# Kernel tuning notes

Hardware: AMD Instinct MI355X
Metric: run time of the kernel (lower is better)

Reference implementation:

```python
import jax, jax.numpy as jnp
import numpy as np

L = 1024       # qlen
B = 2          # batch
D = 1024       # hidden_size
NH = 16        # heads
DH = 64        # d_head
NL = 4         # num_hidden_layers
MLEN = 1024    # memory length
KLEN = MLEN + L


def setup_inputs() -> dict:
    key = jax.random.key(0)
    ks = jax.random.split(key, 10)
    s = 0.02
    # causal mask: key position j is masked (True) if j > mlen + i
    attn_mask = (jnp.arange(KLEN)[None, :] > (MLEN + jnp.arange(L))[:, None])[:, :, None]
    return {
        "mems": jax.random.normal(ks[0], (NL + 1, MLEN, B, D), jnp.float32),
        "raw_embeddings": jax.random.normal(ks[1], (L, B, D), jnp.float32),
        "attention_mask": attn_mask,
        "r_w_bias": jax.random.normal(ks[2], (NH, DH), jnp.float32) * s,
        "r_r_bias": jax.random.normal(ks[3], (NH, DH), jnp.float32) * s,
        "qkv_w": jax.random.normal(ks[4], (NL, D, 3 * NH * DH), jnp.float32) * s,
        "r_w": jax.random.normal(ks[5], (NL, D, NH * DH), jnp.float32) * s,
        "o_w": jax.random.normal(ks[6], (NL, NH * DH, D), jnp.float32) * s,
        "ln1_g": jnp.ones((NL, D), jnp.float32),
        "ln1_b": jnp.zeros((NL, D), jnp.float32),
        "ff_w1": jax.random.normal(ks[7], (NL, D, D), jnp.float32) * s,
        "ff_b1": jnp.zeros((NL, D), jnp.float32),
        "ff_w2": jax.random.normal(ks[8], (NL, D, D), jnp.float32) * s,
        "ff_b2": jnp.zeros((NL, D), jnp.float32),
        "ln2_g": jnp.ones((NL, D), jnp.float32),
        "ln2_b": jnp.zeros((NL, D), jnp.float32),
    }


def _layernorm(x, g, b, eps=1e-5):
    m = jnp.mean(x, axis=-1, keepdims=True)
    v = jnp.var(x, axis=-1, keepdims=True)
    return (x - m) / jnp.sqrt(v + eps) * g + b


def _rel_shift(x):
    # x: (qlen, rlen, b, n) -> XL relative shift via pad/reshape trick
    q, r, b, n = x.shape
    xp = jnp.pad(x, ((0, 0), (1, 0), (0, 0), (0, 0)))     # (q, r+1, b, n)
    xp = xp.reshape(r + 1, q, b, n)                        # flat reinterpret
    return xp[1:].reshape(q, r, b, n)


def _forward(mems, raw_embeddings, attention_mask, r_w_bias, r_r_bias, qkv_w, r_w,
             o_w, ln1_g, ln1_b, ff_w1, ff_b1, ff_w2, ff_b2, ln2_g, ln2_b):
    qlen, bsz, d = raw_embeddings.shape
    mlen = mems.shape[1]
    klen = mlen + qlen
    nh, dh = r_w_bias.shape
    scale = 1.0 / (dh ** 0.5)

    # sinusoidal relative positional embedding: pos_seq = klen-1 ... 0
    pos_seq = jnp.arange(klen - 1, -1, -1, dtype=raw_embeddings.dtype)
    inv_freq = 1.0 / (10000.0 ** (jnp.arange(0, d, 2, dtype=jnp.float32) / d))
    sinusoid = pos_seq[:, None] * inv_freq[None, :]
    pos_emb = jnp.concatenate([jnp.sin(sinusoid), jnp.cos(sinusoid)], axis=-1)  # (klen, D)

    mask = attention_mask[:, :, :, None]  # (L, 2L, 1, 1)
    core = raw_embeddings
    hids = [core]
    n_layers = qkv_w.shape[0]
    for i in range(n_layers):
        cat = jnp.concatenate([mems[i], core], axis=0)          # (klen, b, D)
        w_heads = cat @ qkv_w[i]                                # (klen, b, 3D)
        q, k, v = jnp.split(w_heads, 3, axis=-1)
        q = q[-qlen:]
        q = q.reshape(qlen, bsz, nh, dh)
        k = k.reshape(klen, bsz, nh, dh)
        v = v.reshape(klen, bsz, nh, dh)
        r_head_k = (pos_emb @ r_w[i]).reshape(klen, nh, dh)     # (rlen, n, d)

        AC = jnp.einsum('ibnd,jbnd->ijbn', q + r_w_bias, k)
        BD = _rel_shift(jnp.einsum('ibnd,jnd->ijbn', q + r_r_bias, r_head_k))
        score = (AC + BD) * scale                               # (q, k, b, n)
        score = jnp.where(mask, -jnp.inf, score)
        prob = jax.nn.softmax(score, axis=1)
        attn_vec = jnp.einsum('ijbn,jbnd->ibnd', prob, v).reshape(qlen, bsz, nh * dh)
        attn_out = attn_vec @ o_w[i]
        core = _layernorm(core + attn_out, ln1_g[i], ln1_b[i])  # post-lnorm

        ff = jnp.maximum(core @ ff_w1[i] + ff_b1[i], 0.0) @ ff_w2[i] + ff_b2[i]
        core = _layernorm(core + ff, ln2_g[i], ln2_b[i])
        hids.append(core)

    new_mems = jax.lax.stop_gradient(jnp.stack(hids, axis=0))   # xl_grad=False -> detach
    return core, new_mems


def reference(mems, raw_embeddings, attention_mask, r_w_bias, r_r_bias, qkv_w, r_w,
              o_w, ln1_g, ln1_b, ff_w1, ff_b1, ff_w2, ff_b2, ln2_g, ln2_b):
    return _forward(mems, raw_embeddings, attention_mask, r_w_bias, r_r_bias, qkv_w,
                    r_w, o_w, ln1_g, ln1_b, ff_w1, ff_b1, ff_w2, ff_b2, ln2_g, ln2_b)
```

## Files before the change

### kernel.cpp

```cpp
#include <hip/hip_runtime.h>
#include <hip/hip_bf16.h>

#define QLEN 1024
#define BSZ 2
#define DIM 1024
#define NH 16
#define DH 64
#define NL 4
#define MLEN 1024
#define KLEN 2048
#define QROWS (QLEN*BSZ)
#define CATROWS (KLEN*BSZ)
#define N3 (3*NH*DH)

typedef __hip_bfloat16 bf16;
typedef short bf16x8_t __attribute__((ext_vector_type(8)));
typedef float f32x4_t __attribute__((ext_vector_type(4)));

__device__ __forceinline__ float b2f(bf16 h) { return __bfloat162float(h); }
__device__ __forceinline__ bf16 f2b(float f) { return __float2bfloat16(f); }
__device__ __forceinline__ short f2bs(float f) {
  bf16 h = f2b(f);
  return *reinterpret_cast<short*>(&h);
}

__device__ __forceinline__ float loadf(const void* p, size_t i, int isb) {
  return isb ? b2f(((const bf16*)p)[i]) : ((const float*)p)[i];
}
__device__ __forceinline__ void storef(void* p, size_t i, float v, int isb) {
  if (isb) ((bf16*)p)[i] = f2b(v);
  else     ((float*)p)[i] = v;
}

__device__ __forceinline__ bf16x8_t load_bf8(const bf16* p) {
  union { uint4 u; bf16x8_t v; } x;
  x.u = *reinterpret_cast<const uint4*>(p);
  return x.v;
}

__device__ __forceinline__ void gld_lds16(const bf16* g, bf16* l) {
  __builtin_amdgcn_global_load_lds(
      (const __attribute__((address_space(1))) void*)g,
      (__attribute__((address_space(3))) void*)l, 16, 0, 0);
}

__global__ void probe_kernel(const void* g, int* flag) {
  *flag = (((const unsigned int*)g)[0] == 0x3F803F80u) ? 1 : 0;
}

__global__ void pos_emb_kernel(bf16* __restrict__ pe) {
  int idx = blockIdx.x * 256 + threadIdx.x;
  int j = idx >> 10;
  int c = idx & 1023;
  int fi = (c < 512) ? c : (c - 512);
  float inv = expf(-((float)(2 * fi) * (1.0f / 1024.0f)) * 9.210340371976184f);
  float pos = (float)(KLEN - 1 - j);
  float a = pos * inv;
  float v = (c < 512) ? sinf(a) : cosf(a);
  pe[idx] = f2b(v);
}

__global__ void init_kernel(const void* __restrict__ raw, float* __restrict__ core,
                            void* __restrict__ out, const int* __restrict__ flag) {
  const int isb = *flag;
  int idx = blockIdx.x * 256 + threadIdx.x;
  float v = loadf(raw, idx, isb);
  core[idx] = v;
  storef(out, (size_t)QROWS * DIM + idx, v, isb);
}

__global__ void concat_kernel(const void* __restrict__ mems, size_t memsOff,
                              const float* __restrict__ core,
                              bf16* __restrict__ cat, const int* __restrict__ flag) {
  const int isb = *flag;
  int idx = blockIdx.x * 256 + threadIdx.x;
  const int memElems = MLEN * BSZ * DIM;
  if (idx < memElems) cat[idx] = f2b(loadf(mems, memsOff + idx, isb));
  else                cat[idx] = f2b(core[idx - memElems]);
}

__global__ void transpose5_kernel(const void* __restrict__ qkvw, const void* __restrict__ rw,
                                  const void* __restrict__ ow, const void* __restrict__ ffw1,
                                  const void* __restrict__ ffw2,
                                  bf16* __restrict__ qkvT, bf16* __restrict__ rwT,
                                  bf16* __restrict__ owT, bf16* __restrict__ f1T,
                                  bf16* __restrict__ f2T,
                                  int layer, const int* __restrict__ flag) {
  const int isb = *flag;
  __shared__ float tile[32][33];
  const int n0 = blockIdx.x * 32;
  const int k0 = blockIdx.y * 32;
  const int tx = threadIdx.x & 31;
  const int ty = threadIdx.x >> 5;
  auto doT = [&](const void* W, size_t wOff, bf16* WT, int K, int N) {
    __syncthreads();
#pragma unroll
    for (int r = 0; r < 32; r += 8)
      tile[ty + r][tx] = loadf(W, wOff + (size_t)(k0 + ty + r) * N + n0 + tx, isb);
    __syncthreads();
#pragma unroll
    for (int r = 0; r < 32; r += 8)
      WT[(size_t)(n0 + ty + r) * K + k0 + tx] = f2b(tile[tx][ty + r]);
  };
  doT(qkvw, (size_t)layer * DIM * N3, qkvT, DIM, N3);
  if (n0 < DIM) {
    const size_t o = (size_t)layer * DIM * DIM;
    doT(rw,   o, rwT, DIM, DIM);
    doT(ow,   o, owT, DIM, DIM);
    doT(ffw1, o, f1T, DIM, DIM);
    doT(ffw2, o, f2T, DIM, DIM);
  }
}

template <int EPI, int BM>
__launch_bounds__(256, 2)
__global__ void mgemm_kernel(const bf16* __restrict__ A, const bf16* __restrict__ Bt,
                             float* __restrict__ Cf, bf16* __restrict__ Ch,
                             bf16* __restrict__ Vt,
                             const void* __restrict__ bias, size_t biasOff,
                             int M, int N, int K, const int* __restrict__ flag) {
  const int isb = *flag;
  constexpr int BN = (BM == 128) ? 128 : 64;
  __shared__ bf16 As[BM * 32];
  __shared__ bf16 Bs[BN * 32];
  const int t = threadIdx.x;
  const int wave = t >> 6;
  const int lane = t & 63;
  const int g  = lane >> 4;
  const int lo = lane & 15;
  const int rowA = blockIdx.y * BM;
  const int rowB = blockIdx.x * BN;

  if constexpr (BM == 128) {
    const int wr = wave >> 1, wc = wave & 1;
    const int srow = wave * 32 + (lane >> 2);
    const int scol = (lane & 3) * 8;
    const bf16* gA = A  + (size_t)(rowA + srow) * K + scol;
    const bf16* gB = Bt + (size_t)(rowB + srow) * K + scol;
    bf16* lA = As + wave * 32 * 32;
    bf16* lB = Bs + wave * 32 * 32;

    f32x4_t acc[4][4];
#pragma unroll
    for (int m = 0; m < 4; ++m)
#pragma unroll
      for (int n = 0; n < 4; ++n) acc[m][n] = (f32x4_t){0.f, 0.f, 0.f, 0.f};

    for (int k0 = 0; k0 < K; k0 += 32) {
      gld_lds16(gA + k0, lA);
      gld_lds16(gA + (size_t)16 * K + k0, lA + 16 * 32);
      gld_lds16(gB + k0, lB);
      gld_lds16(gB + (size_t)16 * K + k0, lB + 16 * 32);
      __syncthreads();
      bf16x8_t af[4], bfr[4];
#pragma unroll
      for (int m = 0; m < 4; ++m)
        af[m] = *reinterpret_cast<const bf16x8_t*>(As + (wr * 64 + m * 16 + lo) * 32 + g * 8);
#pragma unroll
      for (int n = 0; n < 4; ++n)
        bfr[n] = *reinterpret_cast<const bf16x8_t*>(Bs + (wc * 64 + n * 16 + lo) * 32 + g * 8);
#pragma unroll
      for (int m = 0; m < 4; ++m)
#pragma unroll
        for (int n = 0; n < 4; ++n)
          acc[m][n] = __builtin_amdgcn_mfma_f32_16x16x32_bf16(af[m], bfr[n], acc[m][n], 0, 0, 0);
      __syncthreads();
    }

#pragma unroll
    for (int m = 0; m < 4; ++m) {
#pragma unroll
      for (int n = 0; n < 4; ++n) {
        const int col = rowB + wc * 64 + n * 16 + lo;
        float bv = 0.f;
        if constexpr (EPI >= 2 && EPI <= 3) bv = loadf(bias, biasOff + col, isb);
#pragma unroll
        for (int r = 0; r < 4; ++r) {
          const int row = rowA + wr * 64 + m * 16 + g * 4 + r;
          float v = acc[m][n][r];
          const size_t o = (size_t)row * N + col;
          if constexpr (EPI == 0)      Cf[o] = v;
          else if constexpr (EPI == 1) Ch[o] = f2b(v);
          else if constexpr (EPI == 2) { v += bv; Ch[o] = f2b(fmaxf(v, 0.f)); }
          else if constexpr (EPI == 3) { v += bv; Cf[o] = v; }
          else {
            if (col < 2 * DIM) Ch[o] = f2b(v);
            else Vt[((size_t)(row & 1) * DIM + (col - 2 * DIM)) * KLEN + (row >> 1)] = f2b(v);
          }
        }
      }
    }
  } else {
    const int srow = t >> 2;
    const int scol = (t & 3) * 8;
    const bf16* gA = A  + (size_t)(rowA + srow) * K + scol;
    const bf16* gB = Bt + (size_t)(rowB + srow) * K + scol;
    bf16* lA = As + wave * 16 * 32;
    bf16* lB = Bs + wave * 16 * 32;

    f32x4_t acc[4];
#pragma unroll
    for (int n = 0; n < 4; ++n) acc[n] = (f32x4_t){0.f, 0.f, 0.f, 0.f};

    for (int k0 = 0; k0 < K; k0 += 32) {
      gld_lds16(gA + k0, lA);
      gld_lds16(gB + k0, lB);
      __syncthreads();
      bf16x8_t af = *reinterpret_cast<const bf16x8_t*>(As + (wave * 16 + lo) * 32 + g * 8);
      bf16x8_t bfr[4];
#pragma unroll
      for (int n = 0; n < 4; ++n)
        bfr[n] = *reinterpret_cast<const bf16x8_t*>(Bs + (n * 16 + lo) * 32 + g * 8);
#pragma unroll
      for (int n = 0; n < 4; ++n)
        acc[n] = __builtin_amdgcn_mfma_f32_16x16x32_bf16(af, bfr[n], acc[n], 0, 0, 0);
      __syncthreads();
    }

#pragma unroll
    for (int n = 0; n < 4; ++n) {
      const int col = rowB + n * 16 + lo;
      float bv = 0.f;
      if constexpr (EPI >= 2) bv = loadf(bias, biasOff + col, isb);
#pragma unroll
      for (int r = 0; r < 4; ++r) {
        const int row = rowA + wave * 16 + g * 4 + r;
        float v = acc[n][r];
        const size_t o = (size_t)row * N + col;
        if constexpr (EPI == 0)      Cf[o] = v;
        else if constexpr (EPI == 1) Ch[o] = f2b(v);
        else if constexpr (EPI == 2) { v += bv; Ch[o] = f2b(fmaxf(v, 0.f)); }
        else if constexpr (EPI == 3) { v += bv; Cf[o] = v; }
      }
    }
  }
}

#define PSTR 56

__launch_bounds__(256)
__global__ void attn_mfma_kernel(const bf16* __restrict__ wh, const bf16* __restrict__ vT,
                                 const bf16* __restrict__ rk,
                                 const void* __restrict__ rwb, const void* __restrict__ rrb,
                                 bf16* __restrict__ av, const int* __restrict__ flag) {
  const int isb = *flag;
  const int bid = blockIdx.x;
  const int x  = bid & 7;
  const int j  = bid >> 3;
  const int head = x * 4 + (j & 3);
  const int b = head >> 4;
  const int n = head & 15;
  const int jj = j >> 2;
  const int qb = (jj < 8) ? jj : 23 - jj;
  const int qbase = qb * 64;
  const int t = threadIdx.x;
  const int wid = t >> 6;
  const int lane = t & 63;
  const int lo = lane & 15;
  const int g  = lane >> 4;
  const int i0 = qbase + wid * 16;

  __shared__ bf16 Kls[2][32 * 64];
  __shared__ bf16 Vtls[2][64 * 32];
  __shared__ bf16 Rls[128 * 64];
  __shared__ short PlsAll[4][16 * PSTR];
  short* Pl = PlsAll[wid];

  const int srow = t >> 3;
  const int kchunk = (t & 7) ^ (srow & 7);
  const size_t rowStride = (size_t)BSZ * N3;
  const bf16* gK  = wh + ((size_t)srow * BSZ + b) * N3 + DIM + n * DH + kchunk * 8;
  const bf16* gVt = vT + ((size_t)b * DIM + n * DH + (t >> 2)) * KLEN
                       + (((t & 3) ^ ((t >> 3) & 3)) << 3);

  auto stageR = [&](int s0) {
    int r = s0 + (t >> 3);
    int rc = (r < KLEN) ? r : (KLEN - 1);
    const bf16* src = rk + (size_t)rc * DIM + n * DH + ((t & 7) ^ ((t >> 3) & 7)) * 8;
    gld_lds16(src, &Rls[(size_t)(s0 & 127) * 64 + (size_t)wid * 512]);
  };

  bf16x8_t qw[2], qr[2];
  {
    const bf16* qrow = wh + ((size_t)(MLEN + i0 + lo) * BSZ + b) * N3 + n * DH;
#pragma unroll
    for (int c = 0; c < 2; ++c) {
      int d0 = c * 32 + g * 8;
#pragma unroll
      for (int jj2 = 0; jj2 < 8; ++jj2) {
        float qv = b2f(qrow[d0 + jj2]);
        qw[c][jj2] = f2bs(qv + loadf(rwb, n * DH + d0 + jj2, isb));
        qr[c][jj2] = f2bs(qv + loadf(rrb, n * DH + d0 + jj2, isb));
      }
    }
  }

  f32x4_t O[4];
  float mrow[4], lrow[4];
#pragma unroll
  for (int d = 0; d < 4; ++d) { O[d] = (f32x4_t){0.f, 0.f, 0.f, 0.f}; }
#pragma unroll
  for (int r = 0; r < 4; ++r) { mrow[r] = -INFINITY; lrow[r] = 0.f; }

  const float SCL = 0.125f * 1.44269504088896f;
  const int jend = MLEN + qbase + 63;

  gld_lds16(gK, &Kls[0][wid * 512]);
  gld_lds16(gVt, &Vtls[0][wid * 512]);
  stageR(MLEN - 64 - qbase);
  stageR(MLEN - 32 - qbase);
  stageR(MLEN - qbase);
  __syncthreads();

  int bi = 0;
  for (int j0 = 0; j0 <= jend; j0 += 32) {
    if (j0 + 32 <= jend) {
      gld_lds16(gK + (size_t)(j0 + 32) * rowStride, &Kls[bi ^ 1][wid * 512]);
      gld_lds16(gVt + j0 + 32, &Vtls[bi ^ 1][wid * 512]);
      stageR(MLEN + 32 + j0 - qbase);
    }
    const bf16* Kl  = Kls[bi];
    const bf16* Vtl = Vtls[bi];

    f32x4_t s[2];
    s[0] = (f32x4_t){0.f, 0.f, 0.f, 0.f};
    s[1] = (f32x4_t){0.f, 0.f, 0.f, 0.f};
#pragma unroll
    for (int c = 0; c < 2; ++c) {
#pragma unroll
      for (int tt = 0; tt < 2; ++tt) {
        const int row = tt * 16 + lo;
        const bf16* kp = Kl + row * 64 + (((c * 4 + g) ^ (row & 7)) << 3);
        s[tt] = __builtin_amdgcn_mfma_f32_16x16x32_bf16(qw[c], load_bf8(kp), s[tt], 0, 0, 0);
      }
    }
    const int u0 = MLEN - 1 + j0 - i0 - 15;
    f32x4_t dacc[3];
    dacc[0] = (f32x4_t){0.f, 0.f, 0.f, 0.f};
    dacc[1] = (f32x4_t){0.f, 0.f, 0.f, 0.f};
    dacc[2] = (f32x4_t){0.f, 0.f, 0.f, 0.f};
#pragma unroll
    for (int c = 0; c < 2; ++c) {
#pragma unroll
      for (int tt = 0; tt < 3; ++tt) {
        const int sr = (u0 + tt * 16 + lo) & 127;
        const bf16* rp = Rls + sr * 64 + (((c * 4 + g) ^ (lo & 7)) << 3);
        dacc[tt] = __builtin_amdgcn_mfma_f32_16x16x32_bf16(qr[c], load_bf8(rp), dacc[tt], 0, 0, 0);
      }
    }

    float sv[2][4];
#pragma unroll
    for (int r = 0; r < 4; ++r) {
      const int ri = g * 4 + r;
      const int srcl = g * 16 + ((lo + 15 - ri) & 15);
      float a0 = __shfl(dacc[0][r], srcl);
      float a1 = __shfl(dacc[1][r], srcl);
      float a2 = __shfl(dacc[2][r], srcl);
      const bool hi = lo > ri;
      float d0 = hi ? a1 : a0;
      float d1 = hi ? a2 : a1;
      bool v0 = (j0 + lo)      <= (MLEN + i0 + ri);
      bool v1 = (j0 + lo + 16) <= (MLEN + i0 + ri);
      sv[0][r] = v0 ? (s[0][r] + d0) * SCL : -INFINITY;
      sv[1][r] = v1 ? (s[1][r] + d1) * SCL : -INFINITY;
    }

    float alpha[4];
#pragma unroll
    for (int r = 0; r < 4; ++r) {
      float v = fmaxf(sv[0][r], sv[1][r]);
      v = fmaxf(v, __shfl_xor(v, 1));
      v = fmaxf(v, __shfl_xor(v, 2));
      v = fmaxf(v, __shfl_xor(v, 4));
      v = fmaxf(v, __shfl_xor(v, 8));
      float mn = fmaxf(mrow[r], v);
      alpha[r] = exp2f(mrow[r] - mn);
      mrow[r] = mn;
    }
    float ps[2][4];
#pragma unroll
    for (int f2 = 0; f2 < 2; ++f2)
#pragma unroll
      for (int r = 0; r < 4; ++r)
        ps[f2][r] = exp2f(sv[f2][r] - mrow[r]);
#pragma unroll
    for (int r = 0; r < 4; ++r) {
      float v = ps[0][r] + ps[1][r];
      v += __shfl_xor(v, 1);
      v += __shfl_xor(v, 2);
      v += __shfl_xor(v, 4);
      v += __shfl_xor(v, 8);
      lrow[r] = lrow[r] * alpha[r] + v;
    }
#pragma unroll
    for (int d = 0; d < 4; ++d)
#pragma unroll
      for (int r = 0; r < 4; ++r)
        O[d][r] *= alpha[r];

#pragma unroll
    for (int f2 = 0; f2 < 2; ++f2)
#pragma unroll
      for (int r = 0; r < 4; ++r)
        Pl[(g * 4 + r) * PSTR + lo + 16 * f2] = f2bs(ps[f2][r]);
    __builtin_amdgcn_wave_barrier();
    bf16x8_t pf = *reinterpret_cast<const bf16x8_t*>(&Pl[lo * PSTR + g * 8]);

#pragma unroll
    for (int dt = 0; dt < 4; ++dt) {
      const int vrow = dt * 16 + lo;
      bf16x8_t vf = load_bf8(Vtl + vrow * 32 + ((g ^ ((lo >> 1) & 3)) << 3));
      O[dt] = __builtin_amdgcn_mfma_f32_16x16x32_bf16(pf, vf, O[dt], 0, 0, 0);
    }

    __syncthreads();
    bi ^= 1;
  }

#pragma unroll
  for (int dt = 0; dt < 4; ++dt)
#pragma unroll
    for (int r = 0; r < 4; ++r) {
      const int ri = g * 4 + r;
      av[((size_t)(i0 + ri) * BSZ + b) * DIM + n * DH + dt * 16 + lo] =
          f2b(O[dt][r] / lrow[r]);
    }
}

template <bool WRITE_HID>
__launch_bounds__(256)
__global__ void resid_ln_kernel(const float* __restrict__ base, const float* __restrict__ add,
                                const void* __restrict__ g, size_t gOff,
                                const void* __restrict__ bta, size_t btaOff,
                                float* __restrict__ core_f, bf16* __restrict__ core_h,
                                void* __restrict__ out, size_t hidOff,
                                const int* __restrict__ flag) {
  const int isb = *flag;
  const int row = blockIdx.x;
  const int t = threadIdx.x;
  __shared__ float red[256];
  __shared__ float red2[256];
  float x[4];
  float s = 0.f, sq = 0.f;
#pragma unroll
  for (int u = 0; u < 4; ++u) {
    int idx = t + u * 256;
    float v = base[(size_t)row * DIM + idx] + add[(size_t)row * DIM + idx];
    x[u] = v; s += v; sq += v * v;
  }
  red[t] = s; red2[t] = sq; __syncthreads();
#pragma unroll
  for (int s2 = 128; s2 > 0; s2 >>= 1) {
    if (t < s2) { red[t] += red[t + s2]; red2[t] += red2[t + s2]; }
    __syncthreads();
  }
  const float mean = red[0] * (1.0f / DIM);
  const float var  = red2[0] * (1.0f / DIM) - mean * mean;
  const float rstd = rsqrtf(var + 1e-5f);
#pragma unroll
  for (int u = 0; u < 4; ++u) {
    int idx = t + u * 256;
    float y = (x[u] - mean) * rstd * loadf(g, gOff + idx, isb) + loadf(bta, btaOff + idx, isb);
    core_f[(size_t)row * DIM + idx] = y;
    core_h[(size_t)row * DIM + idx] = f2b(y);
    if (WRITE_HID) storef(out, hidOff + (size_t)row * DIM + idx, y, isb);
  }
}

__global__ void copy_out_kernel(const float* __restrict__ src, void* __restrict__ out,
                                const int* __restrict__ flag) {
  const int isb = *flag;
  int idx = blockIdx.x * 256 + threadIdx.x;
  storef(out, idx, src[idx], isb);
}

extern "C" void kernel_launch(void* const* d_in, const int* in_sizes, int n_in,
                              void* d_out, int out_size, void* d_ws, size_t ws_size,
                              hipStream_t stream) {
  const void* mems = d_in[0];
  const void* raw  = d_in[1];
  const void* rwb  = d_in[3];
  const void* rrb  = d_in[4];
  const void* qkvw = d_in[5];
  const void* rw   = d_in[6];
  const void* ow   = d_in[7];
  const void* ln1g = d_in[8];
  const void* ln1b = d_in[9];
  const void* ffw1 = d_in[10];
  const void* ffb1 = d_in[11];
  const void* ffw2 = d_in[12];
  const void* ffb2 = d_in[13];
  const void* ln2g = d_in[14];
  const void* ln2b = d_in[15];

  char* w = (char*)d_ws;
  size_t off = 0;
  auto alloc = [&](size_t bytes) -> void* {
    void* p = w + off;
    off += (bytes + 255) & ~(size_t)255;
    return p;
  };
  int*   flag    = (int*)alloc(4);
  bf16*  pos_emb = (bf16*)alloc((size_t)KLEN * DIM * 2);
  bf16*  wh      = (bf16*)alloc((size_t)CATROWS * N3 * 2);
  bf16*  cat     = (bf16*)alloc((size_t)CATROWS * DIM * 2);
  bf16*  rk      = (bf16*)alloc((size_t)KLEN * DIM * 2);
  float* core_f  = (float*)alloc((size_t)QROWS * DIM * 4);
  bf16*  vT      = (bf16*)alloc((size_t)2 * DIM * KLEN * 2);
  bf16*  qkvT    = (bf16*)alloc((size_t)N3 * DIM * 2);
  bf16*  rwT     = (bf16*)alloc((size_t)DIM * DIM * 2);
  bf16*  owT     = (bf16*)alloc((size_t)DIM * DIM * 2);
  bf16*  f1T     = (bf16*)alloc((size_t)DIM * DIM * 2);
  bf16*  f2T     = (bf16*)alloc((size_t)DIM * DIM * 2);
  float* buf1   = (float*)wh;
  bf16*  buf2   = (bf16*)((char*)wh + (size_t)8 * 1024 * 1024);
  bf16*  avec   = cat;
  bf16*  core_h = (bf16*)((char*)cat + (size_t)4 * 1024 * 1024);
  (void)ws_size; (void)in_sizes; (void)n_in; (void)out_size;

  const size_t HID = (size_t)QROWS * DIM;

  probe_kernel<<<1, 1, 0, stream>>>(ln1g, flag);
  pos_emb_kernel<<<KLEN * DIM / 256, 256, 0, stream>>>(pos_emb);
  init_kernel<<<QROWS * DIM / 256, 256, 0, stream>>>(raw, core_f, d_out, flag);

  for (int i = 0; i < NL; ++i) {
    const size_t memsOff = (size_t)i * MLEN * BSZ * DIM;
    transpose5_kernel<<<dim3(96, 32), 256, 0, stream>>>(
        qkvw, rw, ow, ffw1, ffw2, qkvT, rwT, owT, f1T, f2T, i, flag);
    concat_kernel<<<CATROWS * DIM / 256, 256, 0, stream>>>(mems, memsOff, core_f, cat, flag);
    mgemm_kernel<4, 128><<<dim3(N3 / 128, CATROWS / 128), 256, 0, stream>>>(
        cat, qkvT, nullptr, wh, vT, nullptr, 0, CATROWS, N3, DIM, flag);
    mgemm_kernel<1, 64><<<dim3(DIM / 64, KLEN / 64), 256, 0, stream>>>(
        pos_emb, rwT, nullptr, rk, nullptr, nullptr, 0, KLEN, DIM, DIM, flag);
    attn_mfma_kernel<<<512, 256, 0, stream>>>(wh, vT, rk, rwb, rrb, avec, flag);
    mgemm_kernel<0, 64><<<dim3(DIM / 64, QROWS / 64), 256, 0, stream>>>(
        avec, owT, buf1, nullptr, nullptr, nullptr, 0, QROWS, DIM, DIM, flag);
    resid_ln_kernel<false><<<QROWS, 256, 0, stream>>>(
        core_f, buf1, ln1g, (size_t)i * DIM, ln1b, (size_t)i * DIM,
        core_f, core_h, nullptr, 0, flag);
    mgemm_kernel<2, 64><<<dim3(DIM / 64, QROWS / 64), 256, 0, stream>>>(
        core_h, f1T, nullptr, buf2, nullptr, ffb1, (size_t)i * DIM, QROWS, DIM, DIM, flag);
    mgemm_kernel<3, 64><<<dim3(DIM / 64, QROWS / 64), 256, 0, stream>>>(
        buf2, f2T, buf1, nullptr, nullptr, ffb2, (size_t)i * DIM, QROWS, DIM, DIM, flag);
    resid_ln_kernel<true><<<QROWS, 256, 0, stream>>>(
        core_f, buf1, ln2g, (size_t)i * DIM, ln2b, (size_t)i * DIM,
        core_f, core_h, d_out, HID * (size_t)(i + 2), flag);
  }
  copy_out_kernel<<<QROWS * DIM / 256, 256, 0, stream>>>(core_f, d_out, flag);
}
```

Measured before the change: 1.327 ms.

## Split attention over key range into two halves with a separate merge kernel

The attention kernel now splits each query block's key range into two halves (split-K, flash-decoding style). This doubles the grid to 1024 blocks, balances work across them, and raises occupancy via launch bounds. Each half writes unnormalized partial outputs plus its row max and row sum to fp32 scratch. A new merge kernel rescales and combines the two halves into the bf16 attention vector. The cost is an extra kernel launch and extra fp32 traffic for the partial results.

```diff
diff --git a/kernel.cpp b/kernel.cpp
--- a/kernel.cpp
+++ b/kernel.cpp
@@ -238,11 +238,12 @@
 
 #define PSTR 56
 
-__launch_bounds__(256)
+__launch_bounds__(256, 4)
 __global__ void attn_mfma_kernel(const bf16* __restrict__ wh, const bf16* __restrict__ vT,
                                  const bf16* __restrict__ rk,
                                  const void* __restrict__ rwb, const void* __restrict__ rrb,
-                                 bf16* __restrict__ av, const int* __restrict__ flag) {
+                                 float* __restrict__ pO, float* __restrict__ pm,
+                                 float* __restrict__ pl, const int* __restrict__ flag) {
   const int isb = *flag;
   const int bid = blockIdx.x;
   const int x  = bid & 7;
@@ -251,8 +252,13 @@
   const int b = head >> 4;
   const int n = head & 15;
   const int jj = j >> 2;
-  const int qb = (jj < 8) ? jj : 23 - jj;
+  const int kh = jj >> 4;
+  const int s  = jj & 15;
+  const int qb = (s < 8) ? s : 23 - s;
   const int qbase = qb * 64;
+  const int T = 17 + qb;
+  const int jstart = kh * T * 32;
+  const int jlast  = jstart + (T - 1) * 32;
   const int t = threadIdx.x;
   const int wid = t >> 6;
   const int lane = t & 63;
@@ -303,18 +309,17 @@
   for (int r = 0; r < 4; ++r) { mrow[r] = -INFINITY; lrow[r] = 0.f; }
 
   const float SCL = 0.125f * 1.44269504088896f;
-  const int jend = MLEN + qbase + 63;
-
-  gld_lds16(gK, &Kls[0][wid * 512]);
-  gld_lds16(gVt, &Vtls[0][wid * 512]);
-  stageR(MLEN - 64 - qbase);
-  stageR(MLEN - 32 - qbase);
-  stageR(MLEN - qbase);
+
+  gld_lds16(gK + (size_t)jstart * rowStride, &Kls[0][wid * 512]);
+  gld_lds16(gVt + jstart, &Vtls[0][wid * 512]);
+  stageR(MLEN - 64 - qbase + jstart);
+  stageR(MLEN - 32 - qbase + jstart);
+  stageR(MLEN - qbase + jstart);
   __syncthreads();
 
   int bi = 0;
-  for (int j0 = 0; j0 <= jend; j0 += 32) {
-    if (j0 + 32 <= jend) {
+  for (int j0 = jstart; j0 <= jlast; j0 += 32) {
+    if (j0 < jlast) {
       gld_lds16(gK + (size_t)(j0 + 32) * rowStride, &Kls[bi ^ 1][wid * 512]);
       gld_lds16(gVt + j0 + 32, &Vtls[bi ^ 1][wid * 512]);
       stageR(MLEN + 32 + j0 - qbase);
@@ -322,16 +327,16 @@
     const bf16* Kl  = Kls[bi];
     const bf16* Vtl = Vtls[bi];
 
-    f32x4_t s[2];
-    s[0] = (f32x4_t){0.f, 0.f, 0.f, 0.f};
-    s[1] = (f32x4_t){0.f, 0.f, 0.f, 0.f};
+    f32x4_t s2[2];
+    s2[0] = (f32x4_t){0.f, 0.f, 0.f, 0.f};
+    s2[1] = (f32x4_t){0.f, 0.f, 0.f, 0.f};
 #pragma unroll
     for (int c = 0; c < 2; ++c) {
 #pragma unroll
       for (int tt = 0; tt < 2; ++tt) {
         const int row = tt * 16 + lo;
         const bf16* kp = Kl + row * 64 + (((c * 4 + g) ^ (row & 7)) << 3);
-        s[tt] = __builtin_amdgcn_mfma_f32_16x16x32_bf16(qw[c], load_bf8(kp), s[tt], 0, 0, 0);
+        s2[tt] = __builtin_amdgcn_mfma_f32_16x16x32_bf16(qw[c], load_bf8(kp), s2[tt], 0, 0, 0);
       }
     }
     const int u0 = MLEN - 1 + j0 - i0 - 15;
@@ -360,10 +365,10 @@
       const bool hi = lo > ri;
       float d0 = hi ? a1 : a0;
       float d1 = hi ? a2 : a1;
-      bool v0 = (j0 + lo)      <= (MLEN + i0 + ri);
-      bool v1 = (j0 + lo + 16) <= (MLEN + i0 + ri);
-      sv[0][r] = v0 ? (s[0][r] + d0) * SCL : -INFINITY;
-      sv[1][r] = v1 ? (s[1][r] + d1) * SCL : -INFINITY;
+      bool v0 = (kh == 0) || ((j0 + lo)      <= (MLEN + i0 + ri));
+      bool v1 = (kh == 0) || ((j0 + lo + 16) <= (MLEN + i0 + ri));
+      sv[0][r] = v0 ? (s2[0][r] + d0) * SCL : -INFINITY;
+      sv[1][r] = v1 ? (s2[1][r] + d1) * SCL : -INFINITY;
     }
 
     float alpha[4];
@@ -423,9 +428,41 @@
 #pragma unroll
     for (int r = 0; r < 4; ++r) {
       const int ri = g * 4 + r;
-      av[((size_t)(i0 + ri) * BSZ + b) * DIM + n * DH + dt * 16 + lo] =
-          f2b(O[dt][r] / lrow[r]);
-    }
+      pO[((size_t)kh * QROWS + (size_t)(i0 + ri) * BSZ + b) * DIM
+         + n * DH + dt * 16 + lo] = O[dt][r];
+    }
+  if (lo == 0) {
+#pragma unroll
+    for (int r = 0; r < 4; ++r) {
+      const int ri = g * 4 + r;
+      const size_t sidx = (((size_t)kh * BSZ + b) * NH + n) * QLEN + (i0 + ri);
+      pm[sidx] = mrow[r];
+      pl[sidx] = lrow[r];
+    }
+  }
+}
+
+__launch_bounds__(256)
+__global__ void attn_merge_kernel(const float* __restrict__ pO, const float* __restrict__ pm,
+                                  const float* __restrict__ pl, bf16* __restrict__ av) {
+  const int row = blockIdx.x;
+  const int i = row >> 1;
+  const int b = row & 1;
+  const int t = threadIdx.x;
+  const size_t SH = (size_t)BSZ * NH * QLEN;
+#pragma unroll
+  for (int u = 0; u < 4; ++u) {
+    const int d = t + u * 256;
+    const int n = d >> 6;
+    const size_t sidx = ((size_t)b * NH + n) * QLEN + i;
+    const float m0 = pm[sidx], m1 = pm[SH + sidx];
+    const float l0 = pl[sidx], l1 = pl[SH + sidx];
+    const float m = fmaxf(m0, m1);
+    const float c0 = exp2f(m0 - m), c1 = exp2f(m1 - m);
+    const float O0 = pO[(size_t)row * DIM + d];
+    const float O1 = pO[((size_t)QROWS + row) * DIM + d];
+    av[(size_t)row * DIM + d] = f2b((O0 * c0 + O1 * c1) / (l0 * c0 + l1 * c1));
+  }
 }
 
 template <bool WRITE_HID>
@@ -508,6 +545,9 @@
   bf16*  rk      = (bf16*)alloc((size_t)KLEN * DIM * 2);
   float* core_f  = (float*)alloc((size_t)QROWS * DIM * 4);
   bf16*  vT      = (bf16*)alloc((size_t)2 * DIM * KLEN * 2);
+  float* pO      = (float*)alloc((size_t)2 * QROWS * DIM * 4);
+  float* pm      = (float*)alloc((size_t)2 * BSZ * NH * QLEN * 4);
+  float* pl      = (float*)alloc((size_t)2 * BSZ * NH * QLEN * 4);
   bf16*  qkvT    = (bf16*)alloc((size_t)N3 * DIM * 2);
   bf16*  rwT     = (bf16*)alloc((size_t)DIM * DIM * 2);
   bf16*  owT     = (bf16*)alloc((size_t)DIM * DIM * 2);
@@ -534,7 +574,8 @@
         cat, qkvT, nullptr, wh, vT, nullptr, 0, CATROWS, N3, DIM, flag);
     mgemm_kernel<1, 64><<<dim3(DIM / 64, KLEN / 64), 256, 0, stream>>>(
         pos_emb, rwT, nullptr, rk, nullptr, nullptr, 0, KLEN, DIM, DIM, flag);
-    attn_mfma_kernel<<<512, 256, 0, stream>>>(wh, vT, rk, rwb, rrb, avec, flag);
+    attn_mfma_kernel<<<1024, 256, 0, stream>>>(wh, vT, rk, rwb, rrb, pO, pm, pl, flag);
+    attn_merge_kernel<<<QROWS, 256, 0, stream>>>(pO, pm, pl, avec);
     mgemm_kernel<0, 64><<<dim3(DIM / 64, QROWS / 64), 256, 0, stream>>>(
         avec, owT, buf1, nullptr, nullptr, nullptr, 0, QROWS, DIM, DIM, flag);
     resid_ln_kernel<false><<<QROWS, 256, 0, stream>>>(
```

New measurement: 1.248 ms. -5.9%, faster.
